# Kernel tuning notes

Hardware: AMD Instinct MI355X
Metric: run time of the kernel (lower is better)

## Reference

```python
import jax, jax.numpy as jnp
import numpy as np

K_NEIGHBORS = 30
MAX_FLOAT = float(np.finfo(np.float32).max)
DIST_EPS = 1e-6


def setup_inputs() -> dict:
    key = jax.random.key(0)
    k1, k2 = jax.random.split(key)
    # X: (B, N, n_grid_square_types, 3) coordinates; scaled to spread points out
    X = jax.random.normal(k1, (1, 8192, 4, 3), dtype=jnp.float32) * 10.0
    # C: chain/field map; C > 0 means valid node (field_map_to_mask)
    C = jax.random.randint(k2, (1, 8192), 0, 4)
    return {"X": X, "C": C}


def _pairwise_dist(Xc):
    # Xc: (B, N, 3) centroid coordinates -> (B, N, N) Euclidean distances
    sq = jnp.sum(Xc * Xc, axis=-1)                      # (B, N)
    G = jnp.einsum('bnd,bmd->bnm', Xc, Xc)              # Gram matrix (GEMM)
    D2 = sq[:, :, None] + sq[:, None, :] - 2.0 * G
    return jnp.sqrt(jnp.maximum(D2, 0.0) + DIST_EPS)


def reference(X, C):
    # distance_grid_square_type < 0 -> centroid over grid-square types
    Xc = jnp.mean(X, axis=2)                            # (B, N, 3)
    D = _pairwise_dist(Xc)                              # (B, N, N)

    # node mask and 2D edge mask (mask_full = mask_i * mask_j)
    mask_1d = (C > 0).astype(jnp.float32)               # (B, N)
    mask_2d = mask_1d[:, :, None] * mask_1d[:, None, :]  # (B, N, N)

    # masked distances: invalid edges pushed to +max_float
    D_masked = mask_2d * D + (1.0 - mask_2d) * MAX_FLOAT

    # topk smallest distances via top_k on negated values
    neg_vals, edge_idx = jax.lax.top_k(-D_masked, K_NEIGHBORS)
    edge_D = -neg_vals                                  # (B, N, K)

    # graph.collect_edges: gather edge mask at neighbor indices
    mask_ij = jnp.take_along_axis(mask_2d, edge_idx, axis=-1)  # (B, N, K)

    return edge_idx, edge_D, mask_ij
```

## Files before the change

### kernel.cpp

```cpp
#include <hip/hip_runtime.h>
#include <hip/hip_bf16.h>
#include <stdint.h>

typedef unsigned long long u64;
typedef float f32x2 __attribute__((ext_vector_type(2)));

#define N 8192
#define K 30
#define NWAVE 4
#define CAP 576
#define NSLOT 9
#define FLUSH_AT 320


static __device__ __forceinline__ f32x2 pk_mul(f32x2 a, f32x2 b) {
  f32x2 d; asm("v_pk_mul_f32 %0, %1, %2" : "=v"(d) : "v"(a), "v"(b)); return d;
}
static __device__ __forceinline__ f32x2 pk_add(f32x2 a, f32x2 b) {
  f32x2 d; asm("v_pk_add_f32 %0, %1, %2" : "=v"(d) : "v"(a), "v"(b)); return d;
}
static __device__ __forceinline__ f32x2 pk_fma(f32x2 a, f32x2 b, f32x2 c) {
  f32x2 d; asm("v_pk_fma_f32 %0, %1, %2, %3" : "=v"(d) : "v"(a), "v"(b), "v"(c)); return d;
}
static __device__ __forceinline__ f32x2 clamp0(f32x2 a) {
  f32x2 d; d.x = fmaxf(a.x, 0.0f); d.y = fmaxf(a.y, 0.0f); return d;
}

__global__ void zero_kernel(int* __restrict__ ctr) {
  if (threadIdx.x < 2) ctr[threadIdx.x] = 0;
}

__global__ __launch_bounds__(256) void prep_kernel(const float* __restrict__ X,
                                                   const int* __restrict__ C,
                                                   float* __restrict__ gx,
                                                   float* __restrict__ gy,
                                                   float* __restrict__ gz,
                                                   float* __restrict__ gw,
                                                   int* __restrict__ gid,
                                                   int* __restrict__ ctr) {
  int i = blockIdx.x * 256 + threadIdx.x;
  if (i >= N) return;
  const float4* xp = (const float4*)(X + (size_t)i * 12);
  float4 f0 = xp[0], f1 = xp[1], f2 = xp[2];
  float mx = __fmul_rn(__fadd_rn(__fadd_rn(__fadd_rn(f0.x, f0.w), f1.z), f2.y), 0.25f);
  float my = __fmul_rn(__fadd_rn(__fadd_rn(__fadd_rn(f0.y, f1.x), f1.w), f2.z), 0.25f);
  float mz = __fmul_rn(__fadd_rn(__fadd_rn(__fadd_rn(f0.z, f1.y), f2.x), f2.w), 0.25f);
  float sq = __fadd_rn(__fadd_rn(__fmul_rn(mx, mx), __fmul_rn(my, my)), __fmul_rn(mz, mz));
  bool valid = (C[i] > 0);
  int p;
  if (valid) p = atomicAdd(&ctr[0], 1);
  else       p = N - 1 - atomicAdd(&ctr[1], 1);
  gx[p] = mx; gy[p] = my; gz[p] = mz;
  gw[p] = valid ? sq : __builtin_inff();
  gid[p] = i;
}

static __device__ __forceinline__ u64 sort64(u64 v, int lane) {
#pragma unroll
  for (int kk = 2; kk <= 64; kk <<= 1) {
#pragma unroll
    for (int j = kk >> 1; j > 0; j >>= 1) {
      u64 o = __shfl_xor(v, j);
      bool lower = (lane & j) == 0;
      bool asc = (lane & kk) == 0;
      u64 mn = v < o ? v : o;
      u64 mx = v < o ? o : v;
      v = (lower == asc) ? mn : mx;
    }
  }
  return v;
}
static __device__ __forceinline__ u64 merge64(u64 L, u64 v, int lane) {
  u64 vr = __shfl(v, 63 - lane);
  u64 m = L < vr ? L : vr;
#pragma unroll
  for (int j = 32; j > 0; j >>= 1) {
    u64 o = __shfl_xor(m, j);
    bool lower = (lane & j) == 0;
    u64 mn = m < o ? m : o;
    u64 mx = m < o ? o : m;
    m = lower ? mn : mx;
  }
  return m;
}

__device__ __forceinline__ void radix_flush(float& th, unsigned& cnt, u64* bufp,
                                            int lane, u64 lmlt) {
  u64 e[NSLOT];
  unsigned h[NSLOT];
#pragma unroll
  for (int s = 0; s < NSLOT; ++s) {
    e[s] = (unsigned)(lane + 64 * s) < cnt ? bufp[lane + 64 * s] : ~0ull;
    h[s] = (unsigned)(e[s] >> 32);
  }
  unsigned piv = 0;
#pragma unroll
  for (int b = 15; b >= 0; --b) {
    unsigned cand = piv + (0x10000u << b);
    int c = 0;
#pragma unroll
    for (int s = 0; s < NSLOT; ++s) c += __popcll(__ballot(h[s] < cand));
    if (c < K) piv = cand;
  }
  if (piv < 0xFFFF0000u)
    th = fminf(th, __uint_as_float(piv + 0x10000u));

  const unsigned thb = __float_as_uint(th);
  unsigned total = 0;
#pragma unroll
  for (int s = 0; s < NSLOT; ++s) {
    u64 mk = __ballot(h[s] < thb);
    if (mk) {
      unsigned pos = total + (unsigned)__popcll(mk & lmlt);
      if (h[s] < thb) bufp[pos] = e[s];
      total += (unsigned)__popcll(mk);
    }
  }
  cnt = total;
}

__device__ __forceinline__ u64 finalize_row(float& th, unsigned& cnt, u64* bufp,
                                            const int* __restrict__ gid,
                                            int lane, u64 lmlt) {
  radix_flush(th, cnt, bufp, lane, lmlt);
  u64 L = ~0ull;
  for (unsigned base = 0; base < cnt; base += 64) {
    u64 v = ~0ull;
    if (base + (unsigned)lane < cnt) {
      u64 raw = bufp[base + lane];
      float d2c = __uint_as_float((unsigned)(raw >> 32));
      float D = sqrtf(__fadd_rn(d2c, 1e-6f));
      unsigned jo = (unsigned)gid[(unsigned)(raw & 0xFFFFFFFFull)];
      v = ((u64)__float_as_uint(D) << 32) | jo;
    }
    v = sort64(v, lane);
    L = merge64(L, v, lane);
  }
  return L;
}

#define PACK(V, J) (((u64)__float_as_uint(V) << 32) | (unsigned)(J))
#define PROCESS(BUF, CNT, MASK, D2V, JJ)                                       \
  if (MASK) {                                                                  \
    unsigned pos = CNT + (unsigned)__popcll((MASK) & lmlt);                    \
    if (((MASK) >> lane) & 1ull) (BUF)[pos] = PACK(D2V, JJ);                   \
    CNT += (unsigned)__popcll(MASK);                                           \
  }

__device__ __forceinline__ void write_row(int r, bool act, u64 L, int lane,
                                          __hip_bfloat16* __restrict__ out) {
  if (lane >= K) return;
  const int o = r * K + lane;
  if (act) {
    out[o] = __float2bfloat16((float)(unsigned)(L & 0xFFFFFFFFull));
    out[N * K + o] = __float2bfloat16(__uint_as_float((unsigned)(L >> 32)));
    out[2 * N * K + o] = __float2bfloat16(1.0f);
  } else {
    out[o] = __float2bfloat16((float)lane);
    ((unsigned short*)out)[N * K + o] = 0x7F7Fu;
    out[2 * N * K + o] = __float2bfloat16(0.0f);
  }
}

__global__ __launch_bounds__(256) void knn_kernel(const float* __restrict__ gx,
                                                  const float* __restrict__ gy,
                                                  const float* __restrict__ gz,
                                                  const float* __restrict__ gw,
                                                  const int* __restrict__ gid,
                                                  const int* __restrict__ ctr,
                                                  __hip_bfloat16* __restrict__ out) {
  __shared__ u64 bufS[NWAVE][CAP];

  const int lane = threadIdx.x & 63;
  const int w = threadIdx.x >> 6;
  const u64 lmlt = (1ull << lane) - 1ull;
  const int nValid = ctr[0];
  const int pos = blockIdx.x * NWAVE + w;
  const int rout = gid[pos];
  const bool act = pos < nValid;

  if (!act) {
    write_row(rout, false, 0, lane, out);
    return;
  }

  const float qx = gx[pos], qy = gy[pos], qz = gz[pos], qw = gw[pos];
  const f32x2 qx2 = {qx, qx}, qy2 = {qy, qy}, qz2 = {qz, qz}, qw2 = {qw, qw};
  const f32x2 neg1 = {-1.0f, -1.0f};

  float th = __builtin_inff();
  unsigned cnt = 0;
  u64* bp = &bufS[w][0];

  const f32x2* bx = (const f32x2*)gx;
  const f32x2* by = (const f32x2*)gy;
  const f32x2* bz = (const f32x2*)gz;
  const f32x2* bw = (const f32x2*)gw;

  const int niter = (nValid + 255) >> 8;
  int base = 0;
  f32x2 aX = bx[lane], aY = by[lane], aZ = bz[lane], aW = bw[lane];
  f32x2 bX = bx[64 + lane], bY = by[64 + lane], bZ = bz[64 + lane], bW = bw[64 + lane];

#pragma unroll 2
  for (int it = 0; it < niter; ++it) {
    const int nbase = (it < niter - 1) ? base + 128 : base;
    f32x2 naX = bx[nbase + lane], naY = by[nbase + lane];
    f32x2 naZ = bz[nbase + lane], naW = bw[nbase + lane];
    f32x2 nbX = bx[nbase + 64 + lane], nbY = by[nbase + 64 + lane];
    f32x2 nbZ = bz[nbase + 64 + lane], nbW = bw[nbase + 64 + lane];

    f32x2 dotA = pk_add(pk_add(pk_mul(qx2, aX), pk_mul(qy2, aY)), pk_mul(qz2, aZ));
    f32x2 dA = clamp0(pk_fma(pk_add(dotA, dotA), neg1, pk_add(qw2, aW)));
    f32x2 dotB = pk_add(pk_add(pk_mul(qx2, bX), pk_mul(qy2, bY)), pk_mul(qz2, bZ));
    f32x2 dB = clamp0(pk_fma(pk_add(dotB, dotB), neg1, pk_add(qw2, bW)));

    if (it == 0 && nValid >= 256) {
      float l = fminf(fminf(dA.x, dA.y), fminf(dB.x, dB.y));
#pragma unroll
      for (int d = 32; d; d >>= 1) l = fmaxf(l, __shfl_xor(l, d));
      th = l;
    }

    bool pA0 = dA.x <= th, pA1 = dA.y <= th, pB0 = dB.x <= th, pB1 = dB.y <= th;
    u64 mA0 = __ballot(pA0), mA1 = __ballot(pA1);
    u64 mB0 = __ballot(pB0), mB1 = __ballot(pB1);
    if (mA0 | mA1 | mB0 | mB1) {
      const unsigned jA = (unsigned)(2 * (base + lane));
      const unsigned jB = jA + 128;
      PROCESS(bp, cnt, mA0, dA.x, jA)
      PROCESS(bp, cnt, mA1, dA.y, jA + 1)
      PROCESS(bp, cnt, mB0, dB.x, jB)
      PROCESS(bp, cnt, mB1, dB.y, jB + 1)
      if (cnt > FLUSH_AT) radix_flush(th, cnt, bp, lane, lmlt);
    }

    aX = naX; aY = naY; aZ = naZ; aW = naW;
    bX = nbX; bY = nbY; bZ = nbZ; bW = nbW;
    base = nbase;
  }

  u64 L = finalize_row(th, cnt, bp, gid, lane, lmlt);
  write_row(rout, true, L, lane, out);
}

extern "C" void kernel_launch(void* const* d_in, const int* in_sizes, int n_in,
                              void* d_out, int out_size, void* d_ws, size_t ws_size,
                              hipStream_t stream) {
  const float* X = (const float*)d_in[0];
  const int* C = (const int*)d_in[1];
  float* gx = (float*)d_ws;
  float* gy = (float*)((char*)d_ws + 32768);
  float* gz = (float*)((char*)d_ws + 65536);
  float* gw = (float*)((char*)d_ws + 98304);
  int* gid = (int*)((char*)d_ws + 131072);
  int* ctr = (int*)((char*)d_ws + 163840);
  __hip_bfloat16* out = (__hip_bfloat16*)d_out;

  zero_kernel<<<1, 64, 0, stream>>>(ctr);
  prep_kernel<<<N / 256, 256, 0, stream>>>(X, C, gx, gy, gz, gw, gid, ctr);
  knn_kernel<<<N / NWAVE, 256, 0, stream>>>(gx, gy, gz, gw, gid, ctr, out);
}
```

Measured before the change: 66.31 us.

## Process two query rows per wavefront to reuse candidate coordinate loads

Each wavefront now handles two query rows, so every loaded batch of candidate coordinates is used for two distance computations, with separate thresholds, LDS buffers and flushes per row. The loop is manually double-buffered with two register sets (A/B) prefetched two iterations ahead, and the grid shrinks by half. LDS capacity and flush threshold per row are reduced to fit two buffers. This halves global/L2 traffic per row and doubles ILP, at the cost of more registers (possibly lower occupancy) and more frequent flushes.

```diff
diff --git a/kernel.cpp b/kernel.cpp
--- a/kernel.cpp
+++ b/kernel.cpp
@@ -8,9 +8,11 @@
 #define N 8192
 #define K 30
 #define NWAVE 4
-#define CAP 576
-#define NSLOT 9
-#define FLUSH_AT 320
+#define R 2
+#define RPB (NWAVE * R)
+#define NSLOT 7
+#define CAP 448
+#define FLUSH_AT 192
 
 
 static __device__ __forceinline__ f32x2 pk_mul(f32x2 a, f32x2 b) {
@@ -169,28 +171,35 @@
                                                   const int* __restrict__ gid,
                                                   const int* __restrict__ ctr,
                                                   __hip_bfloat16* __restrict__ out) {
-  __shared__ u64 bufS[NWAVE][CAP];
+  __shared__ u64 bufS[NWAVE][R][CAP];
 
   const int lane = threadIdx.x & 63;
   const int w = threadIdx.x >> 6;
   const u64 lmlt = (1ull << lane) - 1ull;
   const int nValid = ctr[0];
-  const int pos = blockIdx.x * NWAVE + w;
-  const int rout = gid[pos];
-  const bool act = pos < nValid;
-
-  if (!act) {
-    write_row(rout, false, 0, lane, out);
+  const int pos0 = blockIdx.x * RPB + w * R;
+  const int rout0 = gid[pos0];
+  const int rout1 = gid[pos0 + 1];
+  const bool a0 = pos0 < nValid;
+  const bool a1 = pos0 + 1 < nValid;
+
+  if (!a0) {
+    write_row(rout0, false, 0, lane, out);
+    write_row(rout1, false, 0, lane, out);
     return;
   }
 
-  const float qx = gx[pos], qy = gy[pos], qz = gz[pos], qw = gw[pos];
-  const f32x2 qx2 = {qx, qx}, qy2 = {qy, qy}, qz2 = {qz, qz}, qw2 = {qw, qw};
+  const float q0x = gx[pos0], q0y = gy[pos0], q0z = gz[pos0], q0w = gw[pos0];
+  const float q1x = gx[pos0 + 1], q1y = gy[pos0 + 1], q1z = gz[pos0 + 1], q1w = gw[pos0 + 1];
+  const f32x2 q0x2 = {q0x, q0x}, q0y2 = {q0y, q0y}, q0z2 = {q0z, q0z}, q0w2 = {q0w, q0w};
+  const f32x2 q1x2 = {q1x, q1x}, q1y2 = {q1y, q1y}, q1z2 = {q1z, q1z}, q1w2 = {q1w, q1w};
   const f32x2 neg1 = {-1.0f, -1.0f};
 
-  float th = __builtin_inff();
-  unsigned cnt = 0;
-  u64* bp = &bufS[w][0];
+  float th0 = __builtin_inff();
+  float th1 = a1 ? __builtin_inff() : -__builtin_inff();
+  unsigned cnt0 = 0, cnt1 = 0;
+  u64* b0 = &bufS[w][0][0];
+  u64* b1 = &bufS[w][1][0];
 
   const f32x2* bx = (const f32x2*)gx;
   const f32x2* by = (const f32x2*)gy;
@@ -198,50 +207,88 @@
   const f32x2* bw = (const f32x2*)gw;
 
   const int niter = (nValid + 255) >> 8;
-  int base = 0;
-  f32x2 aX = bx[lane], aY = by[lane], aZ = bz[lane], aW = bw[lane];
-  f32x2 bX = bx[64 + lane], bY = by[64 + lane], bZ = bz[64 + lane], bW = bw[64 + lane];
-
-#pragma unroll 2
-  for (int it = 0; it < niter; ++it) {
-    const int nbase = (it < niter - 1) ? base + 128 : base;
-    f32x2 naX = bx[nbase + lane], naY = by[nbase + lane];
-    f32x2 naZ = bz[nbase + lane], naW = bw[nbase + lane];
-    f32x2 nbX = bx[nbase + 64 + lane], nbY = by[nbase + 64 + lane];
-    f32x2 nbZ = bz[nbase + 64 + lane], nbW = bw[nbase + 64 + lane];
-
-    f32x2 dotA = pk_add(pk_add(pk_mul(qx2, aX), pk_mul(qy2, aY)), pk_mul(qz2, aZ));
-    f32x2 dA = clamp0(pk_fma(pk_add(dotA, dotA), neg1, pk_add(qw2, aW)));
-    f32x2 dotB = pk_add(pk_add(pk_mul(qx2, bX), pk_mul(qy2, bY)), pk_mul(qz2, bZ));
-    f32x2 dB = clamp0(pk_fma(pk_add(dotB, dotB), neg1, pk_add(qw2, bW)));
-
-    if (it == 0 && nValid >= 256) {
-      float l = fminf(fminf(dA.x, dA.y), fminf(dB.x, dB.y));
-#pragma unroll
-      for (int d = 32; d; d >>= 1) l = fmaxf(l, __shfl_xor(l, d));
-      th = l;
-    }
-
-    bool pA0 = dA.x <= th, pA1 = dA.y <= th, pB0 = dB.x <= th, pB1 = dB.y <= th;
-    u64 mA0 = __ballot(pA0), mA1 = __ballot(pA1);
-    u64 mB0 = __ballot(pB0), mB1 = __ballot(pB1);
-    if (mA0 | mA1 | mB0 | mB1) {
-      const unsigned jA = (unsigned)(2 * (base + lane));
-      const unsigned jB = jA + 128;
-      PROCESS(bp, cnt, mA0, dA.x, jA)
-      PROCESS(bp, cnt, mA1, dA.y, jA + 1)
-      PROCESS(bp, cnt, mB0, dB.x, jB)
-      PROCESS(bp, cnt, mB1, dB.y, jB + 1)
-      if (cnt > FLUSH_AT) radix_flush(th, cnt, bp, lane, lmlt);
-    }
-
-    aX = naX; aY = naY; aZ = naZ; aW = naW;
-    bX = nbX; bY = nbY; bZ = nbZ; bW = nbW;
-    base = nbase;
-  }
-
-  u64 L = finalize_row(th, cnt, bp, gid, lane, lmlt);
-  write_row(rout, true, L, lane, out);
+
+  f32x2 AaX, AaY, AaZ, AaW, AbX, AbY, AbZ, AbW;
+  f32x2 BaX, BaY, BaZ, BaW, BbX, BbY, BbZ, BbW;
+#define LOADS(P, BB)                                                            \
+  P##aX = bx[(BB) + lane]; P##aY = by[(BB) + lane];                             \
+  P##aZ = bz[(BB) + lane]; P##aW = bw[(BB) + lane];                             \
+  P##bX = bx[(BB) + 64 + lane]; P##bY = by[(BB) + 64 + lane];                   \
+  P##bZ = bz[(BB) + 64 + lane]; P##bW = bw[(BB) + 64 + lane];
+
+  LOADS(A, 0)
+  LOADS(B, 128)
+
+#define ITERX(P, IT, PRIME)                                                     \
+  {                                                                             \
+    const int bb = (IT) * 128;                                                  \
+    f32x2 dt0A = pk_add(pk_add(pk_mul(q0x2, P##aX), pk_mul(q0y2, P##aY)),       \
+                        pk_mul(q0z2, P##aZ));                                   \
+    f32x2 d0A = clamp0(pk_fma(pk_add(dt0A, dt0A), neg1, pk_add(q0w2, P##aW)));  \
+    f32x2 dt0B = pk_add(pk_add(pk_mul(q0x2, P##bX), pk_mul(q0y2, P##bY)),       \
+                        pk_mul(q0z2, P##bZ));                                   \
+    f32x2 d0B = clamp0(pk_fma(pk_add(dt0B, dt0B), neg1, pk_add(q0w2, P##bW)));  \
+    f32x2 dt1A = pk_add(pk_add(pk_mul(q1x2, P##aX), pk_mul(q1y2, P##aY)),       \
+                        pk_mul(q1z2, P##aZ));                                   \
+    f32x2 d1A = clamp0(pk_fma(pk_add(dt1A, dt1A), neg1, pk_add(q1w2, P##aW)));  \
+    f32x2 dt1B = pk_add(pk_add(pk_mul(q1x2, P##bX), pk_mul(q1y2, P##bY)),       \
+                        pk_mul(q1z2, P##bZ));                                   \
+    f32x2 d1B = clamp0(pk_fma(pk_add(dt1B, dt1B), neg1, pk_add(q1w2, P##bW)));  \
+    const int pb0 = bb + 256;                                                   \
+    const int pb = pb0 < (N / 2 - 128) ? pb0 : (N / 2 - 128);                   \
+    LOADS(P, pb)                                                                \
+    if (PRIME && nValid >= 256) {                                               \
+      float l0 = fminf(fminf(d0A.x, d0A.y), fminf(d0B.x, d0B.y));               \
+      _Pragma("unroll")                                                         \
+      for (int d = 32; d; d >>= 1) l0 = fmaxf(l0, __shfl_xor(l0, d));           \
+      th0 = l0;                                                                 \
+      if (a1) {                                                                 \
+        float l1 = fminf(fminf(d1A.x, d1A.y), fminf(d1B.x, d1B.y));             \
+        _Pragma("unroll")                                                       \
+        for (int d = 32; d; d >>= 1) l1 = fmaxf(l1, __shfl_xor(l1, d));         \
+        th1 = l1;                                                               \
+      }                                                                         \
+    }                                                                           \
+    bool p00 = d0A.x <= th0, p01 = d0A.y <= th0;                                \
+    bool p02 = d0B.x <= th0, p03 = d0B.y <= th0;                                \
+    bool p10 = d1A.x <= th1, p11 = d1A.y <= th1;                                \
+    bool p12 = d1B.x <= th1, p13 = d1B.y <= th1;                                \
+    u64 m00 = __ballot(p00), m01 = __ballot(p01);                               \
+    u64 m02 = __ballot(p02), m03 = __ballot(p03);                               \
+    u64 m10 = __ballot(p10), m11 = __ballot(p11);                               \
+    u64 m12 = __ballot(p12), m13 = __ballot(p13);                               \
+    const unsigned jA = (unsigned)(2 * (bb + lane));                            \
+    const unsigned jB = jA + 128;                                               \
+    if (m00 | m01 | m02 | m03) {                                                \
+      PROCESS(b0, cnt0, m00, d0A.x, jA)                                         \
+      PROCESS(b0, cnt0, m01, d0A.y, jA + 1)                                     \
+      PROCESS(b0, cnt0, m02, d0B.x, jB)                                         \
+      PROCESS(b0, cnt0, m03, d0B.y, jB + 1)                                     \
+      if (cnt0 > FLUSH_AT) radix_flush(th0, cnt0, b0, lane, lmlt);              \
+    }                                                                           \
+    if (m10 | m11 | m12 | m13) {                                                \
+      PROCESS(b1, cnt1, m10, d1A.x, jA)                                         \
+      PROCESS(b1, cnt1, m11, d1A.y, jA + 1)                                     \
+      PROCESS(b1, cnt1, m12, d1B.x, jB)                                         \
+      PROCESS(b1, cnt1, m13, d1B.y, jB + 1)                                     \
+      if (cnt1 > FLUSH_AT) radix_flush(th1, cnt1, b1, lane, lmlt);              \
+    }                                                                           \
+  }
+
+  ITERX(A, 0, true)
+  int it = 1;
+#pragma unroll 1
+  for (; it + 1 < niter; it += 2) {
+    ITERX(B, it, false)
+    ITERX(A, it + 1, false)
+  }
+  if (it < niter) ITERX(B, it, false)
+
+  u64 L0 = finalize_row(th0, cnt0, b0, gid, lane, lmlt);
+  u64 L1 = a1 ? finalize_row(th1, cnt1, b1, gid, lane, lmlt) : ~0ull;
+
+  write_row(rout0, true, L0, lane, out);
+  write_row(rout1, a1, L1, lane, out);
 }
 
 extern "C" void kernel_launch(void* const* d_in, const int* in_sizes, int n_in,
@@ -259,5 +306,5 @@
 
   zero_kernel<<<1, 64, 0, stream>>>(ctr);
   prep_kernel<<<N / 256, 256, 0, stream>>>(X, C, gx, gy, gz, gw, gid, ctr);
-  knn_kernel<<<N / NWAVE, 256, 0, stream>>>(gx, gy, gz, gw, gid, ctr, out);
-}
+  knn_kernel<<<N / RPB, 256, 0, stream>>>(gx, gy, gz, gw, gid, ctr, out);
+}
```

Measured after the change: 66.45 us. Within noise of the previous version (+0.2%).

## Widen candidate loads to float4 and gate ballots with a per-lane min test

Applied to the files above, without the earlier changes.

The scan loop now loads four candidates per lane per array with 128-bit loads, not two with 64-bit loads, so each step covers 256 points with a single load set. A ping-pong register buffer prefetches two steps ahead. A single ballot on the per-lane minimum now gates the four per-element ballots, skipping them when no lane has a candidate under the threshold. Register pressure rises, and the loop needs explicit peeling, with a clamped prefetch index at the tail.

```diff
diff --git a/kernel.cpp b/kernel.cpp
--- a/kernel.cpp
+++ b/kernel.cpp
@@ -4,12 +4,13 @@
 
 typedef unsigned long long u64;
 typedef float f32x2 __attribute__((ext_vector_type(2)));
+typedef float f32x4 __attribute__((ext_vector_type(4)));
 
 #define N 8192
 #define K 30
 #define NWAVE 4
+#define NSLOT 9
 #define CAP 576
-#define NSLOT 9
 #define FLUSH_AT 320
 
 
@@ -140,12 +141,10 @@
 }
 
 #define PACK(V, J) (((u64)__float_as_uint(V) << 32) | (unsigned)(J))
-#define PROCESS(BUF, CNT, MASK, D2V, JJ)                                       \
-  if (MASK) {                                                                  \
-    unsigned pos = CNT + (unsigned)__popcll((MASK) & lmlt);                    \
-    if (((MASK) >> lane) & 1ull) (BUF)[pos] = PACK(D2V, JJ);                   \
-    CNT += (unsigned)__popcll(MASK);                                           \
-  }
+#define PROC_NB(MASK, PRED, DV, JJ)                                           \
+  { unsigned pos = cnt + (unsigned)__popcll((MASK) & lmlt);                   \
+    if (PRED) bp[pos] = PACK(DV, JJ);                                         \
+    cnt += (unsigned)__popcll(MASK); }
 
 __device__ __forceinline__ void write_row(int r, bool act, u64 L, int lane,
                                           __hip_bfloat16* __restrict__ out) {
@@ -192,53 +191,67 @@
   unsigned cnt = 0;
   u64* bp = &bufS[w][0];
 
-  const f32x2* bx = (const f32x2*)gx;
-  const f32x2* by = (const f32x2*)gy;
-  const f32x2* bz = (const f32x2*)gz;
-  const f32x2* bw = (const f32x2*)gw;
+  const f32x4* bx4 = (const f32x4*)gx;
+  const f32x4* by4 = (const f32x4*)gy;
+  const f32x4* bz4 = (const f32x4*)gz;
+  const f32x4* bw4 = (const f32x4*)gw;
 
   const int niter = (nValid + 255) >> 8;
-  int base = 0;
-  f32x2 aX = bx[lane], aY = by[lane], aZ = bz[lane], aW = bw[lane];
-  f32x2 bX = bx[64 + lane], bY = by[64 + lane], bZ = bz[64 + lane], bW = bw[64 + lane];
-
-#pragma unroll 2
-  for (int it = 0; it < niter; ++it) {
-    const int nbase = (it < niter - 1) ? base + 128 : base;
-    f32x2 naX = bx[nbase + lane], naY = by[nbase + lane];
-    f32x2 naZ = bz[nbase + lane], naW = bw[nbase + lane];
-    f32x2 nbX = bx[nbase + 64 + lane], nbY = by[nbase + 64 + lane];
-    f32x2 nbZ = bz[nbase + 64 + lane], nbW = bw[nbase + 64 + lane];
-
-    f32x2 dotA = pk_add(pk_add(pk_mul(qx2, aX), pk_mul(qy2, aY)), pk_mul(qz2, aZ));
-    f32x2 dA = clamp0(pk_fma(pk_add(dotA, dotA), neg1, pk_add(qw2, aW)));
-    f32x2 dotB = pk_add(pk_add(pk_mul(qx2, bX), pk_mul(qy2, bY)), pk_mul(qz2, bZ));
-    f32x2 dB = clamp0(pk_fma(pk_add(dotB, dotB), neg1, pk_add(qw2, bW)));
-
-    if (it == 0 && nValid >= 256) {
-      float l = fminf(fminf(dA.x, dA.y), fminf(dB.x, dB.y));
-#pragma unroll
-      for (int d = 32; d; d >>= 1) l = fmaxf(l, __shfl_xor(l, d));
-      th = l;
-    }
-
-    bool pA0 = dA.x <= th, pA1 = dA.y <= th, pB0 = dB.x <= th, pB1 = dB.y <= th;
-    u64 mA0 = __ballot(pA0), mA1 = __ballot(pA1);
-    u64 mB0 = __ballot(pB0), mB1 = __ballot(pB1);
-    if (mA0 | mA1 | mB0 | mB1) {
-      const unsigned jA = (unsigned)(2 * (base + lane));
-      const unsigned jB = jA + 128;
-      PROCESS(bp, cnt, mA0, dA.x, jA)
-      PROCESS(bp, cnt, mA1, dA.y, jA + 1)
-      PROCESS(bp, cnt, mB0, dB.x, jB)
-      PROCESS(bp, cnt, mB1, dB.y, jB + 1)
-      if (cnt > FLUSH_AT) radix_flush(th, cnt, bp, lane, lmlt);
-    }
-
-    aX = naX; aY = naY; aZ = naZ; aW = naW;
-    bX = nbX; bY = nbY; bZ = nbZ; bW = nbW;
-    base = nbase;
-  }
+  const int maxb4 = N / 4 - 64;
+
+  f32x4 AX, AY, AZ, AW, BX, BY, BZ, BW;
+#define LOADS(P, B4)                                                           \
+  P##X = bx4[(B4) + lane]; P##Y = by4[(B4) + lane];                            \
+  P##Z = bz4[(B4) + lane]; P##W = bw4[(B4) + lane];
+
+  LOADS(A, 0)
+  LOADS(B, 64)
+
+#define ITERX(P, IT, PRIME)                                                    \
+  {                                                                            \
+    const int bb4 = (IT) * 64;                                                 \
+    f32x2 xlo = {P##X.x, P##X.y}, xhi = {P##X.z, P##X.w};                      \
+    f32x2 ylo = {P##Y.x, P##Y.y}, yhi = {P##Y.z, P##Y.w};                      \
+    f32x2 zlo = {P##Z.x, P##Z.y}, zhi = {P##Z.z, P##Z.w};                      \
+    f32x2 wlo = {P##W.x, P##W.y}, whi = {P##W.z, P##W.w};                      \
+    f32x2 dtl = pk_add(pk_add(pk_mul(qx2, xlo), pk_mul(qy2, ylo)),             \
+                       pk_mul(qz2, zlo));                                      \
+    f32x2 dlo = clamp0(pk_fma(pk_add(dtl, dtl), neg1, pk_add(qw2, wlo)));      \
+    f32x2 dth = pk_add(pk_add(pk_mul(qx2, xhi), pk_mul(qy2, yhi)),             \
+                       pk_mul(qz2, zhi));                                      \
+    f32x2 dhi = clamp0(pk_fma(pk_add(dth, dth), neg1, pk_add(qw2, whi)));      \
+    const int pb4 = (bb4 + 128 < maxb4) ? bb4 + 128 : maxb4;                   \
+    LOADS(P, pb4)                                                              \
+    float mn = fminf(fminf(dlo.x, dlo.y), fminf(dhi.x, dhi.y));                \
+    if (PRIME && nValid >= 256) {                                              \
+      float l = mn;                                                            \
+      _Pragma("unroll")                                                        \
+      for (int d = 32; d; d >>= 1) l = fmaxf(l, __shfl_xor(l, d));             \
+      th = l;          \
+    }                                                                          \
+    u64 anym = __ballot(mn <= th);                                             \
+    if (anym) {                                                                \
+      bool p0 = dlo.x <= th, p1 = dlo.y <= th, p2 = dhi.x <= th, p3 = dhi.y <= th; \
+      u64 m0 = __ballot(p0), m1 = __ballot(p1);                                \
+      u64 m2 = __ballot(p2), m3 = __ballot(p3);                                \
+      const unsigned j0 = (unsigned)(4 * (bb4 + lane));                        \
+      PROC_NB(m0, p0, dlo.x, j0)                                               \
+      PROC_NB(m1, p1, dlo.y, j0 + 1)                                           \
+      PROC_NB(m2, p2, dhi.x, j0 + 2)                                           \
+      PROC_NB(m3, p3, dhi.y, j0 + 3)                                           \
+      if (cnt > FLUSH_AT) radix_flush(th, cnt, bp, lane, lmlt);                \
+    }                                                                          \
+  }
+
+  ITERX(A, 0, true)
+  if (niter > 1) ITERX(B, 1, false)
+  int it = 2;
+#pragma unroll 1
+  for (; it + 1 < niter; it += 2) {
+    ITERX(A, it, false)
+    ITERX(B, it + 1, false)
+  }
+  if (it < niter) ITERX(A, it, false)
 
   u64 L = finalize_row(th, cnt, bp, gid, lane, lmlt);
   write_row(rout, true, L, lane, out);
```

Measured after the change: 56.80 us. -14.3%, faster.
